# Performance work log

Hardware: AMD Instinct MI355X
Metric: run time of the kernel (lower is better)

Reference implementation:

```python
import jax, jax.numpy as jnp
import numpy as np

GROUP_SIZE = 128  # in_features // scales.shape[1]


def setup_inputs() -> dict:
    key = jax.random.key(0)
    kA, kq, ks, kz, kb = jax.random.split(key, 5)
    M, K, N = 2048, 4096, 4096
    G = K // GROUP_SIZE  # 32 groups
    A = jax.random.normal(kA, (M, K), dtype=jnp.float32)
    # unpacked uint4 quantized weights, values in [0, 16)
    qweight = jax.random.randint(kq, (N, K), 0, 16, dtype=jnp.int32)
    # per-group scales (typical GPTQ magnitude) and zero-points (float, 'original' zeros_mode)
    scales = jax.random.uniform(ks, (N, G), dtype=jnp.float32) * 0.02
    zeros = jax.random.uniform(kz, (N, G), dtype=jnp.float32) * 15.0
    bias = jax.random.normal(kb, (N,), dtype=jnp.float32)
    return {"A": A, "qweight": qweight, "scales": scales, "zeros": zeros, "bias": bias}


def reference(A, qweight, scales, zeros, bias):
    # Dequant: W[n,k] = (q[n,k] - zeros[n, k//gs]) * scales[n, k//gs]
    N, K = qweight.shape
    gs = K // scales.shape[1]
    s = jnp.repeat(scales, gs, axis=1)  # [N, K]
    z = jnp.repeat(zeros, gs, axis=1)   # [N, K]
    W = (qweight.astype(A.dtype) - z) * s
    # out[m,n] = sum_k A[m,k] * W[n,k] + bias[n]
    return jnp.einsum("mk,nk->mn", A, W) + bias
```

## Files before the change

kernel.cpp:

```cpp
#include <hip/hip_runtime.h>
#include <cstdint>
#include <cstddef>

#define MM 2048
#define KK 4096
#define NN 4096
#define GG 32
#define BM 128
#define BN 256
#define BK 64
#define NTILES (KK / BK)

typedef _Float16 half8_t __attribute__((ext_vector_type(8)));
typedef _Float16 half4_t __attribute__((ext_vector_type(4)));
typedef float f32x4 __attribute__((ext_vector_type(4)));

__device__ __forceinline__ void load_lds16(const void* gptr, void* lptr) {
  __builtin_amdgcn_global_load_lds(
      (const __attribute__((address_space(1))) unsigned int*)gptr,
      (__attribute__((address_space(3))) unsigned int*)lptr, 16, 0, 0);
}

#define ACNT8 (MM * KK / 8)
__global__ void prep_kernel(const float* __restrict__ A, const int* __restrict__ q,
                            const float* __restrict__ scales, const float* __restrict__ zeros,
                            _Float16* __restrict__ Ah, _Float16* __restrict__ Wh) {
  const int i = blockIdx.x * blockDim.x + threadIdx.x;
  if (i < ACNT8) {
    const float4 v0 = ((const float4*)A)[2 * (size_t)i];
    const float4 v1 = ((const float4*)A)[2 * (size_t)i + 1];
    half8_t h;
    h[0] = (_Float16)v0.x; h[1] = (_Float16)v0.y; h[2] = (_Float16)v0.z; h[3] = (_Float16)v0.w;
    h[4] = (_Float16)v1.x; h[5] = (_Float16)v1.y; h[6] = (_Float16)v1.z; h[7] = (_Float16)v1.w;
    *(half8_t*)(Ah + 8 * (size_t)i) = h;
  } else {
    const int j = i - ACNT8;
    const int e = j << 3;
    const int n = e >> 12;
    const int k = e & (KK - 1);
    const int g = k >> 7;
    const float sc = scales[(n << 5) + g];
    const float zp = zeros[(n << 5) + g];
    const float nzs = -zp * sc;
    const int4 q0 = ((const int4*)q)[2 * (size_t)j];
    const int4 q1 = ((const int4*)q)[2 * (size_t)j + 1];
    half8_t h;
    h[0] = (_Float16)fmaf((float)q0.x, sc, nzs);
    h[1] = (_Float16)fmaf((float)q0.y, sc, nzs);
    h[2] = (_Float16)fmaf((float)q0.z, sc, nzs);
    h[3] = (_Float16)fmaf((float)q0.w, sc, nzs);
    h[4] = (_Float16)fmaf((float)q1.x, sc, nzs);
    h[5] = (_Float16)fmaf((float)q1.y, sc, nzs);
    h[6] = (_Float16)fmaf((float)q1.z, sc, nzs);
    h[7] = (_Float16)fmaf((float)q1.w, sc, nzs);
    *(half8_t*)(Wh + (size_t)e) = h;
  }
}

__global__ __launch_bounds__(512, 2)
void gemm8_kernel(const _Float16* __restrict__ Ah, const _Float16* __restrict__ Wh,
                  const float* __restrict__ bias, float* __restrict__ out)
{
  __shared__ __align__(16) _Float16 sA0[BM * BK], sA1[BM * BK], sA2[BM * BK];
  __shared__ __align__(16) _Float16 sB0[BN * BK], sB1[BN * BK], sB2[BN * BK];

  const int tid = threadIdx.x;
  const int lane = tid & 63;
  const int wave = tid >> 6;
  const int wr = wave >> 2;
  const int wc = wave & 3;
  const int lr = lane & 15, quad = lane >> 4;

  const int bid = blockIdx.x;
  const int xcd = bid & 7;
  const int slot = bid >> 3;
  const int mt = slot >> 1;
  const int nt = xcd * 2 + (slot & 1);
  const int m0 = mt * BM;
  const int n0 = nt * BN;

  const int srow = lane >> 3, scc = lane & 7, gch = scc ^ srow;

  f32x4 acc[4][4];
#pragma unroll
  for (int i = 0; i < 4; ++i)
#pragma unroll
    for (int j = 0; j < 4; ++j) acc[i][j] = (f32x4){0.f, 0.f, 0.f, 0.f};

#define STAGE_A(dst, t, i)                                                          \
  load_lds16(Ah + (size_t)(m0 + (i) * 64 + (wave << 3) + srow) * KK + (t) * BK + (gch << 3), \
             (void*)&dst[((i) * 64 + (wave << 3)) * BK])
#define STAGE_B(dst, t, i)                                                          \
  load_lds16(Wh + (size_t)(n0 + (i) * 64 + (wave << 3) + srow) * KK + (t) * BK + (gch << 3), \
             (void*)&dst[((i) * 64 + (wave << 3)) * BK])

#define TILE_BODY(pAb, pBb, nAb, nBb, T)                                            \
  do {                                                                              \
    const int t_ = (T);                                                             \
    const bool st_ = (t_ + 2 < NTILES);                                \
    half8_t a0_[2][2], a1_[2][2], b_[4][2];                                         \
    _Pragma("unroll")                                                               \
    for (int x = 0; x < 2; ++x) {                                                   \
      const _Float16* ba = &pAb[(wr * 64 + x * 16 + lr) * BK];                      \
      _Pragma("unroll")                                                             \
      for (int ks = 0; ks < 2; ++ks)                                                \
        a0_[x][ks] = *(const half8_t*)&ba[((ks * 4 + quad) ^ (lr & 7)) * 8];        \
    }                                                                               \
    _Pragma("unroll")                                                               \
    for (int ni = 0; ni < 4; ++ni) {                                                \
      const _Float16* bb = &pBb[(wc * 64 + ni * 16 + lr) * BK];                     \
      _Pragma("unroll")                                                             \
      for (int ks = 0; ks < 2; ++ks)                                                \
        b_[ni][ks] = *(const half8_t*)&bb[((ks * 4 + quad) ^ (lr & 7)) * 8];        \
    }                                                                               \
    if (st_) { STAGE_B(nBb, t_ + 2, 0); STAGE_B(nBb, t_ + 2, 1); STAGE_A(nAb, t_ + 2, 0); } \
    __builtin_amdgcn_sched_barrier(0);                                              \
    __builtin_amdgcn_s_barrier();                                                   \
    __builtin_amdgcn_s_setprio(1);                                                  \
    _Pragma("unroll")                                                               \
    for (int x = 0; x < 2; ++x)                                                     \
      _Pragma("unroll")                                                             \
      for (int ni = 0; ni < 4; ++ni) {                                              \
        acc[x][ni] = __builtin_amdgcn_mfma_f32_16x16x32_f16(a0_[x][0], b_[ni][0], acc[x][ni], 0, 0, 0); \
        acc[x][ni] = __builtin_amdgcn_mfma_f32_16x16x32_f16(a0_[x][1], b_[ni][1], acc[x][ni], 0, 0, 0); \
      }                                                                             \
    __builtin_amdgcn_s_setprio(0);                                                  \
    __builtin_amdgcn_s_barrier();                                                   \
    _Pragma("unroll")                                                               \
    for (int x = 0; x < 2; ++x) {                                                   \
      const _Float16* ba = &pAb[(wr * 64 + (x + 2) * 16 + lr) * BK];                \
      _Pragma("unroll")                                                             \
      for (int ks = 0; ks < 2; ++ks)                                                \
        a1_[x][ks] = *(const half8_t*)&ba[((ks * 4 + quad) ^ (lr & 7)) * 8];        \
    }                                                                               \
    if (st_) { STAGE_B(nBb, t_ + 2, 2); STAGE_B(nBb, t_ + 2, 3); STAGE_A(nAb, t_ + 2, 1); } \
    __builtin_amdgcn_sched_barrier(0);                                              \
    __builtin_amdgcn_s_barrier();                                                   \
    __builtin_amdgcn_s_setprio(1);                                                  \
    _Pragma("unroll")                                                               \
    for (int x = 0; x < 2; ++x)                                                     \
      _Pragma("unroll")                                                             \
      for (int ni = 0; ni < 4; ++ni) {                                              \
        acc[x + 2][ni] = __builtin_amdgcn_mfma_f32_16x16x32_f16(a1_[x][0], b_[ni][0], acc[x + 2][ni], 0, 0, 0); \
        acc[x + 2][ni] = __builtin_amdgcn_mfma_f32_16x16x32_f16(a1_[x][1], b_[ni][1], acc[x + 2][ni], 0, 0, 0); \
      }                                                                             \
    __builtin_amdgcn_s_setprio(0);                                                  \
    if (t_ < NTILES - 2) asm volatile("s_waitcnt vmcnt(6)" ::: "memory");           \
    else                 asm volatile("s_waitcnt vmcnt(0)" ::: "memory");           \
    __builtin_amdgcn_s_barrier();                                                   \
  } while (0)

  STAGE_B(sB0, 0, 0); STAGE_B(sB0, 0, 1); STAGE_A(sA0, 0, 0);
  STAGE_B(sB0, 0, 2); STAGE_B(sB0, 0, 3); STAGE_A(sA0, 0, 1);
  STAGE_B(sB1, 1, 0); STAGE_B(sB1, 1, 1); STAGE_A(sA1, 1, 0);
  STAGE_B(sB1, 1, 2); STAGE_B(sB1, 1, 3); STAGE_A(sA1, 1, 1);
  asm volatile("s_waitcnt vmcnt(6)" ::: "memory");
  __builtin_amdgcn_s_barrier();

  for (int tt = 0; tt < 63; tt += 3) {
    TILE_BODY(sA0, sB0, sA2, sB2, tt);
    TILE_BODY(sA1, sB1, sA0, sB0, tt + 1);
    TILE_BODY(sA2, sB2, sA1, sB1, tt + 2);
  }
  TILE_BODY(sA0, sB0, sA2, sB2, 63);

#undef TILE_BODY
#undef STAGE_A
#undef STAGE_B

#pragma unroll
  for (int ni = 0; ni < 4; ++ni) {
    const int n = n0 + wc * 64 + ni * 16 + lr;
    const float bv = bias[n];
#pragma unroll
    for (int mi = 0; mi < 4; ++mi) {
      const int mbase = m0 + wr * 64 + mi * 16 + quad * 4;
#pragma unroll
      for (int r = 0; r < 4; ++r)
        out[(size_t)(mbase + r) * NN + n] = acc[mi][ni][r] + bv;
    }
  }
}

__global__ __launch_bounds__(256, 2)
void gemm_fused_kernel(const float* __restrict__ Af, const int* __restrict__ qw,
                       const float* __restrict__ scales, const float* __restrict__ zeros,
                       const float* __restrict__ bias, float* __restrict__ out)
{
  __shared__ __align__(16) _Float16 sA[128 * 64];
  __shared__ __align__(16) _Float16 sB[128 * 64];

  const int tid = threadIdx.x;
  const int lane = tid & 63;
  const int wave = tid >> 6;
  const int wr = wave >> 1, wc = wave & 1;

  const int bid = blockIdx.x;
  const int xcd = bid & 7;
  const int slot = bid >> 3;
  const int mt = slot >> 2;
  const int nt = xcd * 4 + (slot & 3);
  const int m0 = mt * 128;
  const int n0 = nt * 128;

  const int lr = lane & 15, quad = lane >> 4;

  f32x4 acc[4][4];
#pragma unroll
  for (int i = 0; i < 4; ++i)
#pragma unroll
    for (int j = 0; j < 4; ++j) acc[i][j] = (f32x4){0.f, 0.f, 0.f, 0.f};

  const int frow = tid >> 4;
  const int fc4 = tid & 15;

  for (int kt = 0; kt < KK / 64; ++kt) {
    const int k0 = kt * 64;
    const int g = k0 >> 7;
#pragma unroll
    for (int p = 0; p < 8; ++p) {
      const int row = p * 16 + frow;
      const int pc = (fc4 >> 1) ^ (row & 7);
      const int dst = row * 64 + pc * 8 + (fc4 & 1) * 4;
      const float4 avf = *(const float4*)&Af[(size_t)(m0 + row) * KK + k0 + fc4 * 4];
      half4_t ah;
      ah[0] = (_Float16)avf.x; ah[1] = (_Float16)avf.y;
      ah[2] = (_Float16)avf.z; ah[3] = (_Float16)avf.w;
      *(half4_t*)&sA[dst] = ah;
      const int n = n0 + row;
      const float sc = scales[(n << 5) + g];
      const float zp = zeros[(n << 5) + g];
      const float nzs = -zp * sc;
      const int4 qv = *(const int4*)&qw[(size_t)n * KK + k0 + fc4 * 4];
      half4_t bh;
      bh[0] = (_Float16)fmaf((float)qv.x, sc, nzs);
      bh[1] = (_Float16)fmaf((float)qv.y, sc, nzs);
      bh[2] = (_Float16)fmaf((float)qv.z, sc, nzs);
      bh[3] = (_Float16)fmaf((float)qv.w, sc, nzs);
      *(half4_t*)&sB[dst] = bh;
    }
    __syncthreads();
#pragma unroll
    for (int ks = 0; ks < 2; ++ks) {
      half8_t a[4], b[4];
#pragma unroll
      for (int t = 0; t < 4; ++t) {
        const int rA = wr * 64 + t * 16 + lr;
        const int j = ks * 4 + quad;
        a[t] = *(const half8_t*)&sA[rA * 64 + ((j ^ (lr & 7)) * 8)];
        const int rB = wc * 64 + t * 16 + lr;
        b[t] = *(const half8_t*)&sB[rB * 64 + ((j ^ (lr & 7)) * 8)];
      }
#pragma unroll
      for (int mi = 0; mi < 4; ++mi)
#pragma unroll
        for (int ni = 0; ni < 4; ++ni)
          acc[mi][ni] = __builtin_amdgcn_mfma_f32_16x16x32_f16(a[mi], b[ni], acc[mi][ni], 0, 0, 0);
    }
    __syncthreads();
  }

#pragma unroll
  for (int ni = 0; ni < 4; ++ni) {
    const int n = n0 + wc * 64 + ni * 16 + lr;
    const float bv = bias[n];
#pragma unroll
    for (int mi = 0; mi < 4; ++mi) {
      const int mbase = m0 + wr * 64 + mi * 16 + quad * 4;
#pragma unroll
      for (int r = 0; r < 4; ++r)
        out[(size_t)(mbase + r) * NN + n] = acc[mi][ni][r] + bv;
    }
  }
}

extern "C" void kernel_launch(void* const* d_in, const int* in_sizes, int n_in,
                              void* d_out, int out_size, void* d_ws, size_t ws_size,
                              hipStream_t stream) {
  (void)in_sizes; (void)n_in; (void)out_size;
  const float* A      = (const float*)d_in[0];
  const int*   qw     = (const int*)d_in[1];
  const float* scales = (const float*)d_in[2];
  const float* zeros  = (const float*)d_in[3];
  const float* bias   = (const float*)d_in[4];
  float* out = (float*)d_out;

  const size_t needA = (size_t)MM * KK * sizeof(_Float16);
  const size_t needW = (size_t)NN * KK * sizeof(_Float16);

  if (ws_size >= needA + needW) {
    _Float16* Ah = (_Float16*)d_ws;
    _Float16* Wh = (_Float16*)((char*)d_ws + needA);
    prep_kernel<<<((MM + NN) * KK / 8) / 256, 256, 0, stream>>>(A, qw, scales, zeros, Ah, Wh);
    gemm8_kernel<<<dim3(MM / BM * NN / BN), dim3(512), 0, stream>>>(Ah, Wh, bias, out);
  } else {
    gemm_fused_kernel<<<dim3(512), dim3(256), 0, stream>>>(A, qw, scales, zeros, bias, out);
  }
}
```

Before: 214.3 us.

## Split K across wave halves in gemm8 with LDS reduction of partial sums

Reorganizes the 8 waves of the fp16 MFMA GEMM so that each pair of wave groups splits the BK=64 tile along K (kh), with each wave covering a 64x128 output sub-tile instead of 64x64. Each wave now loads 4 A fragments plus 8 B fragments per tile instead of 4 A plus 4 B at double K depth, which cuts LDS read traffic per MFMA. The cost is twice the accumulator registers (acc[4][8]) and an epilogue where the kh=1 waves write partials to LDS and the kh=0 waves add them before storing. This raises register pressure under launch_bounds(512,2) and adds extra barriers at the end.

```diff
diff --git a/kernel.cpp b/kernel.cpp
--- a/kernel.cpp
+++ b/kernel.cpp
@@ -67,8 +67,9 @@
   const int tid = threadIdx.x;
   const int lane = tid & 63;
   const int wave = tid >> 6;
-  const int wr = wave >> 2;
-  const int wc = wave & 3;
+  const int kh = wave >> 2;
+  const int wc = (wave >> 1) & 1;
+  const int wr = wave & 1;
   const int lr = lane & 15, quad = lane >> 4;
 
   const int bid = blockIdx.x;
@@ -81,11 +82,11 @@
 
   const int srow = lane >> 3, scc = lane & 7, gch = scc ^ srow;
 
-  f32x4 acc[4][4];
+  f32x4 acc[4][8];
 #pragma unroll
   for (int i = 0; i < 4; ++i)
 #pragma unroll
-    for (int j = 0; j < 4; ++j) acc[i][j] = (f32x4){0.f, 0.f, 0.f, 0.f};
+    for (int j = 0; j < 8; ++j) acc[i][j] = (f32x4){0.f, 0.f, 0.f, 0.f};
 
 #define STAGE_A(dst, t, i)                                                          \
   load_lds16(Ah + (size_t)(m0 + (i) * 64 + (wave << 3) + srow) * KK + (t) * BK + (gch << 3), \
@@ -98,52 +99,39 @@
   do {                                                                              \
     const int t_ = (T);                                                             \
     const bool st_ = (t_ + 2 < NTILES);                                \
-    half8_t a0_[2][2], a1_[2][2], b_[4][2];                                         \
-    _Pragma("unroll")                                                               \
-    for (int x = 0; x < 2; ++x) {                                                   \
-      const _Float16* ba = &pAb[(wr * 64 + x * 16 + lr) * BK];                      \
-      _Pragma("unroll")                                                             \
-      for (int ks = 0; ks < 2; ++ks)                                                \
-        a0_[x][ks] = *(const half8_t*)&ba[((ks * 4 + quad) ^ (lr & 7)) * 8];        \
-    }                                                                               \
-    _Pragma("unroll")                                                               \
-    for (int ni = 0; ni < 4; ++ni) {                                                \
-      const _Float16* bb = &pBb[(wc * 64 + ni * 16 + lr) * BK];                     \
-      _Pragma("unroll")                                                             \
-      for (int ks = 0; ks < 2; ++ks)                                                \
-        b_[ni][ks] = *(const half8_t*)&bb[((ks * 4 + quad) ^ (lr & 7)) * 8];        \
-    }                                                                               \
+    half8_t a_[4], b_[4], c_[4];                                                    \
+    _Pragma("unroll")                                                               \
+    for (int x = 0; x < 4; ++x)                                                     \
+      a_[x] = *(const half8_t*)&pAb[(wr * 64 + x * 16 + lr) * BK +                  \
+                                    (((kh * 4 + quad) ^ (lr & 7)) * 8)];            \
+    _Pragma("unroll")                                                               \
+    for (int x = 0; x < 4; ++x)                                                     \
+      b_[x] = *(const half8_t*)&pBb[(wc * 128 + x * 16 + lr) * BK +                 \
+                                    (((kh * 4 + quad) ^ (lr & 7)) * 8)];            \
     if (st_) { STAGE_B(nBb, t_ + 2, 0); STAGE_B(nBb, t_ + 2, 1); STAGE_A(nAb, t_ + 2, 0); } \
     __builtin_amdgcn_sched_barrier(0);                                              \
     __builtin_amdgcn_s_barrier();                                                   \
     __builtin_amdgcn_s_setprio(1);                                                  \
     _Pragma("unroll")                                                               \
-    for (int x = 0; x < 2; ++x)                                                     \
+    for (int mi = 0; mi < 4; ++mi)                                                  \
       _Pragma("unroll")                                                             \
-      for (int ni = 0; ni < 4; ++ni) {                                              \
-        acc[x][ni] = __builtin_amdgcn_mfma_f32_16x16x32_f16(a0_[x][0], b_[ni][0], acc[x][ni], 0, 0, 0); \
-        acc[x][ni] = __builtin_amdgcn_mfma_f32_16x16x32_f16(a0_[x][1], b_[ni][1], acc[x][ni], 0, 0, 0); \
-      }                                                                             \
+      for (int ni = 0; ni < 4; ++ni)                                                \
+        acc[mi][ni] = __builtin_amdgcn_mfma_f32_16x16x32_f16(a_[mi], b_[ni], acc[mi][ni], 0, 0, 0); \
     __builtin_amdgcn_s_setprio(0);                                                  \
     __builtin_amdgcn_s_barrier();                                                   \
     _Pragma("unroll")                                                               \
-    for (int x = 0; x < 2; ++x) {                                                   \
-      const _Float16* ba = &pAb[(wr * 64 + (x + 2) * 16 + lr) * BK];                \
-      _Pragma("unroll")                                                             \
-      for (int ks = 0; ks < 2; ++ks)                                                \
-        a1_[x][ks] = *(const half8_t*)&ba[((ks * 4 + quad) ^ (lr & 7)) * 8];        \
-    }                                                                               \
+    for (int x = 0; x < 4; ++x)                                                     \
+      c_[x] = *(const half8_t*)&pBb[(wc * 128 + (x + 4) * 16 + lr) * BK +           \
+                                    (((kh * 4 + quad) ^ (lr & 7)) * 8)];            \
     if (st_) { STAGE_B(nBb, t_ + 2, 2); STAGE_B(nBb, t_ + 2, 3); STAGE_A(nAb, t_ + 2, 1); } \
     __builtin_amdgcn_sched_barrier(0);                                              \
     __builtin_amdgcn_s_barrier();                                                   \
     __builtin_amdgcn_s_setprio(1);                                                  \
     _Pragma("unroll")                                                               \
-    for (int x = 0; x < 2; ++x)                                                     \
+    for (int mi = 0; mi < 4; ++mi)                                                  \
       _Pragma("unroll")                                                             \
-      for (int ni = 0; ni < 4; ++ni) {                                              \
-        acc[x + 2][ni] = __builtin_amdgcn_mfma_f32_16x16x32_f16(a1_[x][0], b_[ni][0], acc[x + 2][ni], 0, 0, 0); \
-        acc[x + 2][ni] = __builtin_amdgcn_mfma_f32_16x16x32_f16(a1_[x][1], b_[ni][1], acc[x + 2][ni], 0, 0, 0); \
-      }                                                                             \
+      for (int ni = 0; ni < 4; ++ni)                                                \
+        acc[mi][ni + 4] = __builtin_amdgcn_mfma_f32_16x16x32_f16(a_[mi], c_[ni], acc[mi][ni + 4], 0, 0, 0); \
     __builtin_amdgcn_s_setprio(0);                                                  \
     if (t_ < NTILES - 2) asm volatile("s_waitcnt vmcnt(6)" ::: "memory");           \
     else                 asm volatile("s_waitcnt vmcnt(0)" ::: "memory");           \
@@ -168,16 +156,36 @@
 #undef STAGE_A
 #undef STAGE_B
 
-#pragma unroll
-  for (int ni = 0; ni < 4; ++ni) {
-    const int n = n0 + wc * 64 + ni * 16 + lr;
-    const float bv = bias[n];
-#pragma unroll
-    for (int mi = 0; mi < 4; ++mi) {
-      const int mbase = m0 + wr * 64 + mi * 16 + quad * 4;
-#pragma unroll
-      for (int r = 0; r < 4; ++r)
-        out[(size_t)(mbase + r) * NN + n] = acc[mi][ni][r] + bv;
+  {
+    float* rbuf = (wave & 2) ? (float*)sB1 : (float*)sB0;
+    float* base = rbuf + ((wave & 1) * 64 + lane) * 64;
+#pragma unroll
+    for (int r = 0; r < 2; ++r) {
+      if (kh == 1) {
+#pragma unroll
+        for (int mi = 0; mi < 4; ++mi)
+#pragma unroll
+          for (int nj = 0; nj < 4; ++nj)
+            *(f32x4*)&base[(mi * 4 + nj) * 4] = acc[mi][r * 4 + nj];
+      }
+      __syncthreads();
+      if (kh == 0) {
+#pragma unroll
+        for (int nj = 0; nj < 4; ++nj) {
+          const int ni = r * 4 + nj;
+          const int n = n0 + wc * 128 + ni * 16 + lr;
+          const float bv = bias[n];
+#pragma unroll
+          for (int mi = 0; mi < 4; ++mi) {
+            const f32x4 p = *(const f32x4*)&base[(mi * 4 + nj) * 4];
+            const int mbase = m0 + wr * 64 + mi * 16 + quad * 4;
+#pragma unroll
+            for (int rr = 0; rr < 4; ++rr)
+              out[(size_t)(mbase + rr) * NN + n] = acc[mi][ni][rr] + p[rr] + bv;
+          }
+        }
+      }
+      __syncthreads();
     }
   }
 }
```

Result: no change. 215.0 us (+0.4%).
